# Kernel tuning notes

Hardware: AMD Instinct MI355X
Metric: run time of the kernel (lower is better)

The kernel has to match this reference:

```python
import jax, jax.numpy as jnp
import numpy as np

D = 128
N_DRUG = 100000
N_PROT = 50000
E_DD, E_DP, E_PD = 800000, 600000, 600000
EPS = 1e-5


def setup_inputs() -> dict:
    key = jax.random.key(0)
    ks = jax.random.split(key, 19)
    f32 = jnp.float32
    return {
        "x_drug": jax.random.normal(ks[0], (N_DRUG, D), f32),
        "x_prot": jax.random.normal(ks[1], (N_PROT, D), f32),
        "Wagg_dd": jax.random.normal(ks[2], (D, D), f32) * 0.05,
        "Wagg_dp": jax.random.normal(ks[3], (D, D), f32) * 0.05,
        "Wagg_pd": jax.random.normal(ks[4], (D, D), f32) * 0.05,
        "W_drug": jax.random.normal(ks[5], (D, 2 * D), f32) * 0.05,
        "b_drug": jax.random.normal(ks[6], (D,), f32) * 0.01,
        "W_prot": jax.random.normal(ks[7], (D, 2 * D), f32) * 0.05,
        "b_prot": jax.random.normal(ks[8], (D,), f32) * 0.01,
        "g_drug": jnp.ones((D,), f32),
        "be_drug": jnp.zeros((D,), f32),
        "g_prot": jnp.ones((D,), f32),
        "be_prot": jnp.zeros((D,), f32),
        "ei_dd_src": jax.random.randint(ks[9], (E_DD,), 0, N_DRUG, jnp.int64 if jax.config.jax_enable_x64 else jnp.int32),
        "ei_dd_dst": jax.random.randint(ks[10], (E_DD,), 0, N_DRUG),
        "ei_dp_src": jax.random.randint(ks[11], (E_DP,), 0, N_DRUG),
        "ei_dp_dst": jax.random.randint(ks[12], (E_DP,), 0, N_PROT),
        "ei_pd_src": jax.random.randint(ks[13], (E_PD,), 0, N_PROT),
        "ei_pd_dst": jax.random.randint(ks[14], (E_PD,), 0, N_DRUG),
    }


def _rel_agg(x_src, W_agg, src_idx, dst_idx, n_dst):
    # gather -> per-relation Linear (no bias) + ReLU -> scatter-mean
    h = jax.nn.relu(x_src[src_idx] @ W_agg.T)            # [E, D]
    s = jax.ops.segment_sum(h, dst_idx, num_segments=n_dst)
    c = jax.ops.segment_sum(jnp.ones((src_idx.shape[0],), h.dtype), dst_idx, num_segments=n_dst)
    return s / jnp.maximum(c, 1.0)[:, None]


def _layernorm(x, g, b):
    mu = jnp.mean(x, axis=-1, keepdims=True)
    var = jnp.mean(jnp.square(x - mu), axis=-1, keepdims=True)
    return (x - mu) * jax.lax.rsqrt(var + EPS) * g + b


def _node_update(h_self, h_agg, W, b, g, be):
    h = jax.nn.relu(jnp.concatenate([h_self, h_agg], axis=-1) @ W.T + b)
    return _layernorm(h + h_self, g, be)  # dropout is identity in eval


def reference(x_drug, x_prot, Wagg_dd, Wagg_dp, Wagg_pd, W_drug, b_drug,
              W_prot, b_prot, g_drug, be_drug, g_prot, be_prot,
              ei_dd_src, ei_dd_dst, ei_dp_src, ei_dp_dst, ei_pd_src, ei_pd_dst):
    agg_dd = _rel_agg(x_drug, Wagg_dd, ei_dd_src, ei_dd_dst, N_DRUG)
    agg_pd = _rel_agg(x_prot, Wagg_pd, ei_pd_src, ei_pd_dst, N_DRUG)
    agg_drug = (agg_dd + agg_pd) * 0.5                   # mean over relations into 'drug'
    agg_prot = _rel_agg(x_drug, Wagg_dp, ei_dp_src, ei_dp_dst, N_PROT)
    out_drug = _node_update(x_drug, agg_drug, W_drug, b_drug, g_drug, be_drug)
    out_prot = _node_update(x_prot, agg_prot, W_prot, b_prot, g_prot, be_prot)
    # pack the per-type outputs into one array [N_DRUG + N_PROT, D]
    return jnp.concatenate([out_drug, out_prot], axis=0)
```

## Files before the change

kernel.cpp:

```cpp
#include <hip/hip_runtime.h>

#define D 128
#define ND 100000
#define NP 50000
#define NE_DD 800000
#define NE_DP 600000
#define NE_PD 600000
#define NE_TOT 2000000

#define NTOT 250000
#define NBC 490
#define NC 250880
#define CHUNKA 4096
#define NBLKA 489
#define CHUNKIT 16
#define SEGCAP 8192

#define TF_BD 782
#define TF_BP 196
#define NU_BD 391
#define NU_BP 196

typedef __bf16 bf16;
typedef __attribute__((ext_vector_type(8))) __bf16 bf16x8;
typedef __attribute__((ext_vector_type(2))) __bf16 bf16x2;
typedef __attribute__((ext_vector_type(4))) float f32x4;
typedef __attribute__((ext_vector_type(2))) float f32x2;

#define OFF_WDD   0UL
#define OFF_WDP   32768UL
#define OFF_WPD   65536UL
#define OFF_WDRUG 98304UL
#define OFF_WPROT 163840UL
#define OFF_YDD   229376UL
#define OFF_YDP   (OFF_YDD + 25600000UL)
#define OFF_YPD   (OFF_YDP + 25600000UL)
#define OFF_AGGD  (OFF_YPD + 12800000UL)
#define OFF_AGGP  (OFF_AGGD + 25600000UL)
#define OFF_BCNT  (OFF_AGGP + 12800000UL)
#define OFF_GCUR  (OFF_BCNT + 2048UL)
#define OFF_CBASE (OFF_GCUR + 2048UL)
#define OFF_RP    (OFF_CBASE + 2048UL)
#define OFF_PAIRS (OFF_RP + 1003520UL)
#define OFF_POOL  (OFF_PAIRS + 16000000UL)

__global__ __launch_bounds__(256) void prep_kernel(
    const float* __restrict__ w0, const float* __restrict__ w1,
    const float* __restrict__ w2, const float* __restrict__ w3,
    const float* __restrict__ w4,
    bf16* __restrict__ o0, bf16* __restrict__ o1, bf16* __restrict__ o2,
    bf16* __restrict__ o3, bf16* __restrict__ o4,
    int* __restrict__ bcnt)
{
    int m = blockIdx.y;
    int i = blockIdx.x * 256 + threadIdx.x;
    if (m == 5) {
        if (i < NBC) bcnt[i] = 0;
        return;
    }
    const float* src; bf16* dst; int n; bool perm;
    switch (m) {
        case 0: src = w0; dst = o0; n = D * D; perm = false; break;
        case 1: src = w1; dst = o1; n = D * D; perm = false; break;
        case 2: src = w2; dst = o2; n = D * D; perm = false; break;
        case 3: src = w3; dst = o3; n = D * 2 * D; perm = true; break;
        default: src = w4; dst = o4; n = D * 2 * D; perm = true; break;
    }
    if (i < n) {
        int si = i;
        if (perm) {
            int col = i & 255;
            if (col >= 128) {
                int p = col - 128;
                si = (i & ~255) | (128 + (p & 7) * 16 + (p >> 3));
            }
        }
        dst[i] = (bf16)src[si];
    }
}


__device__ __forceinline__ bf16x8 load_a_f32(const float* __restrict__ xr)
{
    float4 f0 = *(const float4*)xr;
    float4 f1 = *(const float4*)(xr + 4);
    bf16x8 a;
    a[0] = (bf16)f0.x; a[1] = (bf16)f0.y; a[2] = (bf16)f0.z; a[3] = (bf16)f0.w;
    a[4] = (bf16)f1.x; a[5] = (bf16)f1.y; a[6] = (bf16)f1.z; a[7] = (bf16)f1.w;
    return a;
}

__device__ __forceinline__ void transform_drug(
    const float* __restrict__ x, const bf16* __restrict__ W1,
    const bf16* __restrict__ W2, bf16* __restrict__ y1, bf16* __restrict__ y2,
    int blk)
{
    int lane = threadIdx.x & 63;
    int wave = threadIdx.x >> 6;
    int q = lane >> 4, c = lane & 15;
    int mb = blk * 128 + wave * 32;

    f32x4 acc1[2][8], acc2[2][8];
#pragma unroll
    for (int mt = 0; mt < 2; mt++)
#pragma unroll
        for (int nt = 0; nt < 8; nt++) { acc1[mt][nt] = 0; acc2[mt][nt] = 0; }

#pragma unroll
    for (int kb = 0; kb < 4; kb++) {
        int k = kb * 32 + q * 8;
        bf16x8 a[2];
#pragma unroll
        for (int mt = 0; mt < 2; mt++) {
            int row = min(mb + mt * 16 + c, ND - 1);
            a[mt] = load_a_f32(x + (long)row * D + k);
        }
#pragma unroll
        for (int nt = 0; nt < 8; nt++) {
            bf16x8 b1 = *(const bf16x8*)(W1 + (nt * 16 + c) * D + k);
            bf16x8 b2 = *(const bf16x8*)(W2 + (nt * 16 + c) * D + k);
#pragma unroll
            for (int mt = 0; mt < 2; mt++) {
                acc1[mt][nt] = __builtin_amdgcn_mfma_f32_16x16x32_bf16(a[mt], b1, acc1[mt][nt], 0, 0, 0);
                acc2[mt][nt] = __builtin_amdgcn_mfma_f32_16x16x32_bf16(a[mt], b2, acc2[mt][nt], 0, 0, 0);
            }
        }
    }
#pragma unroll
    for (int mt = 0; mt < 2; mt++)
#pragma unroll
        for (int r = 0; r < 4; r++) {
            int row = mb + mt * 16 + q * 4 + r;
            if (row < ND) {
                bf16x8 o1, o2;
#pragma unroll
                for (int nt = 0; nt < 8; nt++) {
                    o1[nt] = (bf16)fmaxf(acc1[mt][nt][r], 0.f);
                    o2[nt] = (bf16)fmaxf(acc2[mt][nt][r], 0.f);
                }
                *(bf16x8*)(y1 + (long)row * D + c * 8) = o1;
                *(bf16x8*)(y2 + (long)row * D + c * 8) = o2;
            }
        }
}

__device__ __forceinline__ void transform_prot(
    const float* __restrict__ x, const bf16* __restrict__ W1,
    bf16* __restrict__ y1, int blk)
{
    int lane = threadIdx.x & 63;
    int wave = threadIdx.x >> 6;
    int q = lane >> 4, c = lane & 15;
    int mb = blk * 256 + wave * 64;

    f32x4 acc[4][8];
#pragma unroll
    for (int mt = 0; mt < 4; mt++)
#pragma unroll
        for (int nt = 0; nt < 8; nt++) acc[mt][nt] = 0;

#pragma unroll
    for (int kb = 0; kb < 4; kb++) {
        int k = kb * 32 + q * 8;
        bf16x8 a[4];
#pragma unroll
        for (int mt = 0; mt < 4; mt++) {
            int row = min(mb + mt * 16 + c, NP - 1);
            a[mt] = load_a_f32(x + (long)row * D + k);
        }
#pragma unroll
        for (int nt = 0; nt < 8; nt++) {
            bf16x8 b1 = *(const bf16x8*)(W1 + (nt * 16 + c) * D + k);
#pragma unroll
            for (int mt = 0; mt < 4; mt++)
                acc[mt][nt] = __builtin_amdgcn_mfma_f32_16x16x32_bf16(a[mt], b1, acc[mt][nt], 0, 0, 0);
        }
    }
#pragma unroll
    for (int mt = 0; mt < 4; mt++)
#pragma unroll
        for (int r = 0; r < 4; r++) {
            int row = mb + mt * 16 + q * 4 + r;
            if (row < NP) {
                bf16x8 o1;
#pragma unroll
                for (int nt = 0; nt < 8; nt++)
                    o1[nt] = (bf16)fmaxf(acc[mt][nt][r], 0.f);
                *(bf16x8*)(y1 + (long)row * D + c * 8) = o1;
            }
        }
}

__global__ __launch_bounds__(256, 2) void transform_kernel(
    const float* __restrict__ x_drug, const float* __restrict__ x_prot,
    const bf16* __restrict__ Wdd, const bf16* __restrict__ Wdp,
    const bf16* __restrict__ Wpd,
    bf16* __restrict__ y_dd, bf16* __restrict__ y_dp, bf16* __restrict__ y_pd)
{
    int blk = blockIdx.x;
    if (blk < TF_BD)
        transform_drug(x_drug, Wdd, Wdp, y_dd, y_dp, blk);
    else
        transform_prot(x_prot, Wpd, y_pd, blk - TF_BD);
}

__global__ __launch_bounds__(256) void hist_kernel(
    const int* __restrict__ dd_dst, const int* __restrict__ pd_dst,
    const int* __restrict__ dp_dst, int* __restrict__ bcnt)
{
    __shared__ int h[NBC];
    for (int i = threadIdx.x; i < NBC; i += 256) h[i] = 0;
    __syncthreads();
    int base = blockIdx.x * CHUNKA;
    for (int it = 0; it < CHUNKIT; it++) {
        int e = base + it * 256 + threadIdx.x;
        if (e < NE_TOT) {
            int didx;
            if (e < NE_DD) didx = dd_dst[e];
            else if (e < NE_DD + NE_PD) didx = ND + pd_dst[e - NE_DD];
            else didx = 2 * ND + dp_dst[e - NE_DD - NE_PD];
            atomicAdd(&h[didx >> 9], 1);
        }
    }
    __syncthreads();
    for (int i = threadIdx.x; i < NBC; i += 256)
        if (h[i]) atomicAdd(&bcnt[i], h[i]);
}

__global__ __launch_bounds__(256) void scan_kernel(
    const int* __restrict__ bcnt, int* __restrict__ cbase, int* __restrict__ gcur)
{
    __shared__ int ps[256];
    int t = threadIdx.x;
    int i0 = 2 * t, i1 = 2 * t + 1;
    int c0 = (i0 < NBC) ? bcnt[i0] : 0;
    int c1 = (i1 < NBC) ? bcnt[i1] : 0;
    ps[t] = c0 + c1;
    __syncthreads();
#pragma unroll
    for (int off = 1; off < 256; off <<= 1) {
        int add = (t >= off) ? ps[t - off] : 0;
        __syncthreads();
        ps[t] += add;
        __syncthreads();
    }
    int excl = ps[t] - (c0 + c1);
    if (i0 <= NBC) cbase[i0] = excl;
    if (i0 < NBC) gcur[i0] = excl;
    if (i1 < NBC) { cbase[i1] = excl + c0; gcur[i1] = excl + c0; }
}

__global__ __launch_bounds__(256) void binA_kernel(
    const int* __restrict__ dd_src, const int* __restrict__ dd_dst,
    const int* __restrict__ pd_src, const int* __restrict__ pd_dst,
    const int* __restrict__ dp_src, const int* __restrict__ dp_dst,
    int* __restrict__ gcur, int2* __restrict__ pairs)
{
    __shared__ int h[NBC];
    __shared__ int gb[NBC];
    __shared__ int2 pr[CHUNKA];
    __shared__ unsigned short rk[CHUNKA];
    for (int i = threadIdx.x; i < NBC; i += 256) h[i] = 0;
    __syncthreads();
    int base = blockIdx.x * CHUNKA;
    for (int it = 0; it < CHUNKIT; it++) {
        int idx = it * 256 + threadIdx.x;
        int e = base + idx;
        int didx = -1, sv = 0;
        if (e < NE_TOT) {
            if (e < NE_DD) { didx = dd_dst[e]; sv = dd_src[e]; }
            else if (e < NE_DD + NE_PD) { int u = e - NE_DD; didx = ND + pd_dst[u]; sv = pd_src[u]; }
            else { int u = e - NE_DD - NE_PD; didx = 2 * ND + dp_dst[u]; sv = dp_src[u]; }
            rk[idx] = (unsigned short)atomicAdd(&h[didx >> 9], 1);
        }
        pr[idx] = make_int2(didx, sv);
    }
    __syncthreads();
    for (int b = threadIdx.x; b < NBC; b += 256) {
        int c = h[b];
        gb[b] = c ? atomicAdd(&gcur[b], c) : 0;
    }
    __syncthreads();
    for (int it = 0; it < CHUNKIT; it++) {
        int idx = it * 256 + threadIdx.x;
        int2 p = pr[idx];
        if (p.x >= 0) pairs[gb[p.x >> 9] + rk[idx]] = p;
    }
}

__global__ __launch_bounds__(256) void sortB_kernel(
    const int* __restrict__ cbase, const int2* __restrict__ pairs,
    int* __restrict__ pool, int* __restrict__ rp)
{
    __shared__ int h[512];
    __shared__ int excl[512];
    __shared__ int ps[256];
    __shared__ unsigned short rk[SEGCAP];
    __shared__ int outl[SEGCAP];

    int b = blockIdx.x;
    int s0 = cbase[b], s1 = cbase[b + 1];
    int n = s1 - s0;
    if (n > SEGCAP) n = SEGCAP;
    int t = threadIdx.x;
    h[t] = 0; h[t + 256] = 0;
    __syncthreads();

    for (int i = t; i < n; i += 256) {
        int2 p = pairs[s0 + i];
        rk[i] = (unsigned short)atomicAdd(&h[p.x & 511], 1);
    }
    __syncthreads();

    int c0 = h[2 * t], c1 = h[2 * t + 1];
    ps[t] = c0 + c1;
    __syncthreads();
#pragma unroll
    for (int off = 1; off < 256; off <<= 1) {
        int add = (t >= off) ? ps[t - off] : 0;
        __syncthreads();
        ps[t] += add;
        __syncthreads();
    }
    int pe = ps[t] - (c0 + c1);
    excl[2 * t] = pe;
    excl[2 * t + 1] = pe + c0;
    __syncthreads();

    int nb = b * 512;
    rp[nb + 2 * t] = s0 + excl[2 * t];
    rp[nb + 2 * t + 1] = s0 + excl[2 * t + 1];

    for (int i = t; i < n; i += 256) {
        int2 p = pairs[s0 + i];
        outl[excl[p.x & 511] + rk[i]] = p.y;
    }
    __syncthreads();
    for (int i = t; i < n; i += 256)
        pool[s0 + i] = outl[i];
}

__device__ __forceinline__ void acc2(unsigned u, f32x2* acc)
{
    union { unsigned u; float f; } lo, hi;
    lo.u = u << 16;
    hi.u = u & 0xFFFF0000u;
    f32x2 d; d.x = lo.f; d.y = hi.f;
    *acc += d;
}

__device__ __forceinline__ void acc_seg(
    const int* __restrict__ pool, int s, int e,
    const unsigned* __restrict__ y, int lane, f32x2* acc)
{
    int j = s;
    for (; j + 8 <= e; j += 8) {
        unsigned u[8];
#pragma unroll
        for (int t = 0; t < 8; t++)
            u[t] = y[(long)pool[j + t] * 64 + lane];
#pragma unroll
        for (int t = 0; t < 8; t++) acc2(u[t], acc);
    }
    if (j + 4 <= e) {
        unsigned u[4];
#pragma unroll
        for (int t = 0; t < 4; t++)
            u[t] = y[(long)pool[j + t] * 64 + lane];
#pragma unroll
        for (int t = 0; t < 4; t++) acc2(u[t], acc);
        j += 4;
    }
    if (j + 2 <= e) {
        unsigned u0 = y[(long)pool[j] * 64 + lane];
        unsigned u1 = y[(long)pool[j + 1] * 64 + lane];
        acc2(u0, acc); acc2(u1, acc);
        j += 2;
    }
    if (j < e)
        acc2(y[(long)pool[j] * 64 + lane], acc);
}

__global__ __launch_bounds__(256) void gather_kernel(
    const int* __restrict__ rp, const int* __restrict__ pool,
    const unsigned* __restrict__ y_dd, const unsigned* __restrict__ y_pd,
    const unsigned* __restrict__ y_dp,
    bf16* __restrict__ agg_d, bf16* __restrict__ agg_p)
{
    int wid = blockIdx.x * 4 + (threadIdx.x >> 6);
    int lane = threadIdx.x & 63;

    if (wid < ND) {
        int g = wid;
        int s1 = rp[g], e1 = rp[g + 1];
        int s2 = rp[ND + g], e2 = rp[ND + g + 1];
        f32x2 a; a.x = 0.f; a.y = 0.f;
        f32x2 b; b.x = 0.f; b.y = 0.f;
        acc_seg(pool, s1, e1, y_dd, lane, &a);
        acc_seg(pool, s2, e2, y_pd, lane, &b);
        float i1 = 0.5f / (float)max(e1 - s1, 1);
        float i2 = 0.5f / (float)max(e2 - s2, 1);
        f32x2 r = a * i1 + b * i2;
        bf16x2 o; o[0] = (bf16)r.x; o[1] = (bf16)r.y;
        *(bf16x2*)(agg_d + (long)g * D + lane * 2) = o;
    } else if (wid < ND + NP) {
        int p = wid - ND;
        int s1 = rp[2 * ND + p], e1 = rp[2 * ND + p + 1];
        f32x2 a; a.x = 0.f; a.y = 0.f;
        acc_seg(pool, s1, e1, y_dp, lane, &a);
        float i1 = 1.0f / (float)max(e1 - s1, 1);
        f32x2 r = a * i1;
        bf16x2 o; o[0] = (bf16)r.x; o[1] = (bf16)r.y;
        *(bf16x2*)(agg_p + (long)p * D + lane * 2) = o;
    }
}

__device__ __forceinline__ void node_update_body(
    const float* __restrict__ x, const bf16* __restrict__ agg,
    const bf16* __restrict__ W, const float* __restrict__ b,
    const float* __restrict__ g, const float* __restrict__ be,
    float* __restrict__ out, int M, int blk)
{
    int lane = threadIdx.x & 63;
    int wave = threadIdx.x >> 6;
    int q = lane >> 4, c = lane & 15;
    int mb = blk * 256 + wave * 64;

    f32x4 acc[4][8];
#pragma unroll
    for (int mt = 0; mt < 4; mt++)
#pragma unroll
        for (int nt = 0; nt < 8; nt++) acc[mt][nt] = 0;

#pragma unroll
    for (int kb = 0; kb < 8; kb++) {
        bf16x8 a[4];
#pragma unroll
        for (int mt = 0; mt < 4; mt++) {
            int row = min(mb + mt * 16 + c, M - 1);
            if (kb < 4)
                a[mt] = load_a_f32(x + (long)row * D + kb * 32 + q * 8);
            else
                a[mt] = *(const bf16x8*)(agg + (long)row * D + (kb - 4) * 32 + q * 8);
        }
#pragma unroll
        for (int nt = 0; nt < 8; nt++) {
            bf16x8 bw = *(const bf16x8*)(W + (nt * 16 + c) * (2 * D) + kb * 32 + q * 8);
#pragma unroll
            for (int mt = 0; mt < 4; mt++)
                acc[mt][nt] = __builtin_amdgcn_mfma_f32_16x16x32_bf16(a[mt], bw, acc[mt][nt], 0, 0, 0);
        }
    }

    float bv[8], gv[8], bev[8];
#pragma unroll
    for (int nt = 0; nt < 8; nt++) {
        int col = nt * 16 + c;
        bv[nt] = b[col]; gv[nt] = g[col]; bev[nt] = be[col];
    }
#pragma unroll
    for (int mt = 0; mt < 4; mt++)
#pragma unroll
        for (int r = 0; r < 4; r++) {
            int row = mb + mt * 16 + q * 4 + r;
            int rowc = min(row, M - 1);
            const float* xr = x + (long)rowc * D + c;
            float v[8];
            float sum = 0.f, sq = 0.f;
#pragma unroll
            for (int nt = 0; nt < 8; nt++) {
                float h = fmaxf(acc[mt][nt][r] + bv[nt], 0.f);
                float t = h + xr[nt * 16];
                v[nt] = t; sum += t; sq += t * t;
            }
#pragma unroll
            for (int m = 1; m < 16; m <<= 1) {
                sum += __shfl_xor(sum, m, 64);
                sq  += __shfl_xor(sq,  m, 64);
            }
            float mu   = sum * (1.f / 128.f);
            float var  = sq  * (1.f / 128.f) - mu * mu;
            float rstd = rsqrtf(var + 1e-5f);
            if (row < M) {
                float* op = out + (long)row * D + c;
#pragma unroll
                for (int nt = 0; nt < 8; nt++)
                    op[nt * 16] = (v[nt] - mu) * rstd * gv[nt] + bev[nt];
            }
        }
}

__global__ __launch_bounds__(256, 2) void node_update_kernel(
    const float* __restrict__ x_drug, const float* __restrict__ x_prot,
    const bf16* __restrict__ agg_d, const bf16* __restrict__ agg_p,
    const bf16* __restrict__ Wdrug, const float* __restrict__ b_drug,
    const float* __restrict__ g_drug, const float* __restrict__ be_drug,
    const bf16* __restrict__ Wprot, const float* __restrict__ b_prot,
    const float* __restrict__ g_prot, const float* __restrict__ be_prot,
    float* __restrict__ out)
{
    int blk = blockIdx.x;
    if (blk < NU_BD)
        node_update_body(x_drug, agg_d, Wdrug, b_drug, g_drug, be_drug,
                         out, ND, blk);
    else
        node_update_body(x_prot, agg_p, Wprot, b_prot, g_prot, be_prot,
                         out + (long)ND * D, NP, blk - NU_BD);
}

extern "C" void kernel_launch(void* const* d_in, const int* in_sizes, int n_in,
                              void* d_out, int out_size, void* d_ws, size_t ws_size,
                              hipStream_t stream)
{
    const float* x_drug  = (const float*)d_in[0];
    const float* x_prot  = (const float*)d_in[1];
    const float* Wagg_dd = (const float*)d_in[2];
    const float* Wagg_dp = (const float*)d_in[3];
    const float* Wagg_pd = (const float*)d_in[4];
    const float* W_drug  = (const float*)d_in[5];
    const float* b_drug  = (const float*)d_in[6];
    const float* W_prot  = (const float*)d_in[7];
    const float* b_prot  = (const float*)d_in[8];
    const float* g_drug  = (const float*)d_in[9];
    const float* be_drug = (const float*)d_in[10];
    const float* g_prot  = (const float*)d_in[11];
    const float* be_prot = (const float*)d_in[12];
    const int* dd_src = (const int*)d_in[13];
    const int* dd_dst = (const int*)d_in[14];
    const int* dp_src = (const int*)d_in[15];
    const int* dp_dst = (const int*)d_in[16];
    const int* pd_src = (const int*)d_in[17];
    const int* pd_dst = (const int*)d_in[18];

    char* ws = (char*)d_ws;
    bf16* Wdd   = (bf16*)(ws + OFF_WDD);
    bf16* Wdp   = (bf16*)(ws + OFF_WDP);
    bf16* Wpd   = (bf16*)(ws + OFF_WPD);
    bf16* Wdrug = (bf16*)(ws + OFF_WDRUG);
    bf16* Wprot = (bf16*)(ws + OFF_WPROT);
    bf16* y_dd  = (bf16*)(ws + OFF_YDD);
    bf16* y_dp  = (bf16*)(ws + OFF_YDP);
    bf16* y_pd  = (bf16*)(ws + OFF_YPD);
    bf16* agg_d = (bf16*)(ws + OFF_AGGD);
    bf16* agg_p = (bf16*)(ws + OFF_AGGP);
    int* bcnt   = (int*)(ws + OFF_BCNT);
    int* gcur   = (int*)(ws + OFF_GCUR);
    int* cbase  = (int*)(ws + OFF_CBASE);
    int* rp     = (int*)(ws + OFF_RP);
    int2* pairs = (int2*)(ws + OFF_PAIRS);
    int* pool   = (int*)(ws + OFF_POOL);
    float* out  = (float*)d_out;

    prep_kernel<<<dim3(128, 6), 256, 0, stream>>>(
        Wagg_dd, Wagg_dp, Wagg_pd, W_drug, W_prot,
        Wdd, Wdp, Wpd, Wdrug, Wprot, bcnt);

    transform_kernel<<<TF_BD + TF_BP, 256, 0, stream>>>(
        x_drug, x_prot, Wdd, Wdp, Wpd, y_dd, y_dp, y_pd);

    hist_kernel<<<NBLKA, 256, 0, stream>>>(dd_dst, pd_dst, dp_dst, bcnt);
    scan_kernel<<<1, 256, 0, stream>>>(bcnt, cbase, gcur);
    binA_kernel<<<NBLKA, 256, 0, stream>>>(
        dd_src, dd_dst, pd_src, pd_dst, dp_src, dp_dst, gcur, pairs);
    sortB_kernel<<<NBC, 256, 0, stream>>>(cbase, pairs, pool, rp);

    gather_kernel<<<(ND + NP + 3) / 4, 256, 0, stream>>>(
        rp, pool, (const unsigned*)y_dd, (const unsigned*)y_pd,
        (const unsigned*)y_dp, agg_d, agg_p);

    node_update_kernel<<<NU_BD + NU_BP, 256, 0, stream>>>(
        x_drug, x_prot, agg_d, agg_p,
        Wdrug, b_drug, g_drug, be_drug,
        Wprot, b_prot, g_prot, be_prot, out);
}
```

Baseline: 404.3 us.

## Fuse histogram into prep, co-schedule binning with transform, pack edge pairs

Moves the destination-bucket histogram into the weight-prep kernel (using a grid-stride loop over 128 blocks) and zeroes the bucket counts with a memset. The binning pass and the MFMA feature transform now run as one heterogeneous launch so the memory-bound binning overlaps the compute-bound transform. Edge pairs are packed into a single 32-bit word (low 9 bits of the destination plus a 17-bit source index) instead of int2, halving the intermediate pair traffic. This removes two kernel launches and their serialization, but the shared-memory footprint of the fused kernel may limit occupancy for the transform blocks.

```diff
diff --git a/kernel.cpp b/kernel.cpp
--- a/kernel.cpp
+++ b/kernel.cpp
@@ -50,14 +50,28 @@
     const float* __restrict__ w4,
     bf16* __restrict__ o0, bf16* __restrict__ o1, bf16* __restrict__ o2,
     bf16* __restrict__ o3, bf16* __restrict__ o4,
-    int* __restrict__ bcnt)
+    const int* __restrict__ dd_dst, const int* __restrict__ pd_dst,
+    const int* __restrict__ dp_dst, int* __restrict__ bcnt)
 {
     int m = blockIdx.y;
-    int i = blockIdx.x * 256 + threadIdx.x;
+    int t = threadIdx.x;
     if (m == 5) {
-        if (i < NBC) bcnt[i] = 0;
+        __shared__ int h[NBC];
+        for (int i = t; i < NBC; i += 256) h[i] = 0;
+        __syncthreads();
+        for (int e = blockIdx.x * 256 + t; e < NE_TOT; e += 128 * 256) {
+            int didx;
+            if (e < NE_DD) didx = dd_dst[e];
+            else if (e < NE_DD + NE_PD) didx = ND + pd_dst[e - NE_DD];
+            else didx = 2 * ND + dp_dst[e - NE_DD - NE_PD];
+            atomicAdd(&h[didx >> 9], 1);
+        }
+        __syncthreads();
+        for (int i = t; i < NBC; i += 256)
+            if (h[i]) atomicAdd(&bcnt[i], h[i]);
         return;
     }
+    int i = blockIdx.x * 256 + t;
     const float* src; bf16* dst; int n; bool perm;
     switch (m) {
         case 0: src = w0; dst = o0; n = D * D; perm = false; break;
@@ -79,6 +93,28 @@
     }
 }
 
+__global__ __launch_bounds__(256) void scan_kernel(
+    const int* __restrict__ bcnt, int* __restrict__ cbase, int* __restrict__ gcur)
+{
+    __shared__ int ps[256];
+    int t = threadIdx.x;
+    int i0 = 2 * t, i1 = 2 * t + 1;
+    int c0 = (i0 < NBC) ? bcnt[i0] : 0;
+    int c1 = (i1 < NBC) ? bcnt[i1] : 0;
+    ps[t] = c0 + c1;
+    __syncthreads();
+#pragma unroll
+    for (int off = 1; off < 256; off <<= 1) {
+        int add = (t >= off) ? ps[t - off] : 0;
+        __syncthreads();
+        ps[t] += add;
+        __syncthreads();
+    }
+    int excl = ps[t] - (c0 + c1);
+    if (i0 <= NBC) cbase[i0] = excl;
+    if (i0 < NBC) gcur[i0] = excl;
+    if (i1 < NBC) { cbase[i1] = excl + c0; gcur[i1] = excl + c0; }
+}
 
 __device__ __forceinline__ bf16x8 load_a_f32(const float* __restrict__ xr)
 {
@@ -191,70 +227,12 @@
         }
 }
 
-__global__ __launch_bounds__(256, 2) void transform_kernel(
-    const float* __restrict__ x_drug, const float* __restrict__ x_prot,
-    const bf16* __restrict__ Wdd, const bf16* __restrict__ Wdp,
-    const bf16* __restrict__ Wpd,
-    bf16* __restrict__ y_dd, bf16* __restrict__ y_dp, bf16* __restrict__ y_pd)
-{
-    int blk = blockIdx.x;
-    if (blk < TF_BD)
-        transform_drug(x_drug, Wdd, Wdp, y_dd, y_dp, blk);
-    else
-        transform_prot(x_prot, Wpd, y_pd, blk - TF_BD);
-}
-
-__global__ __launch_bounds__(256) void hist_kernel(
-    const int* __restrict__ dd_dst, const int* __restrict__ pd_dst,
-    const int* __restrict__ dp_dst, int* __restrict__ bcnt)
-{
-    __shared__ int h[NBC];
-    for (int i = threadIdx.x; i < NBC; i += 256) h[i] = 0;
-    __syncthreads();
-    int base = blockIdx.x * CHUNKA;
-    for (int it = 0; it < CHUNKIT; it++) {
-        int e = base + it * 256 + threadIdx.x;
-        if (e < NE_TOT) {
-            int didx;
-            if (e < NE_DD) didx = dd_dst[e];
-            else if (e < NE_DD + NE_PD) didx = ND + pd_dst[e - NE_DD];
-            else didx = 2 * ND + dp_dst[e - NE_DD - NE_PD];
-            atomicAdd(&h[didx >> 9], 1);
-        }
-    }
-    __syncthreads();
-    for (int i = threadIdx.x; i < NBC; i += 256)
-        if (h[i]) atomicAdd(&bcnt[i], h[i]);
-}
-
-__global__ __launch_bounds__(256) void scan_kernel(
-    const int* __restrict__ bcnt, int* __restrict__ cbase, int* __restrict__ gcur)
-{
-    __shared__ int ps[256];
-    int t = threadIdx.x;
-    int i0 = 2 * t, i1 = 2 * t + 1;
-    int c0 = (i0 < NBC) ? bcnt[i0] : 0;
-    int c1 = (i1 < NBC) ? bcnt[i1] : 0;
-    ps[t] = c0 + c1;
-    __syncthreads();
-#pragma unroll
-    for (int off = 1; off < 256; off <<= 1) {
-        int add = (t >= off) ? ps[t - off] : 0;
-        __syncthreads();
-        ps[t] += add;
-        __syncthreads();
-    }
-    int excl = ps[t] - (c0 + c1);
-    if (i0 <= NBC) cbase[i0] = excl;
-    if (i0 < NBC) gcur[i0] = excl;
-    if (i1 < NBC) { cbase[i1] = excl + c0; gcur[i1] = excl + c0; }
-}
-
-__global__ __launch_bounds__(256) void binA_kernel(
+__device__ __forceinline__ void binA_body(
+    int blk,
     const int* __restrict__ dd_src, const int* __restrict__ dd_dst,
     const int* __restrict__ pd_src, const int* __restrict__ pd_dst,
     const int* __restrict__ dp_src, const int* __restrict__ dp_dst,
-    int* __restrict__ gcur, int2* __restrict__ pairs)
+    int* __restrict__ gcur, unsigned* __restrict__ pairs)
 {
     __shared__ int h[NBC];
     __shared__ int gb[NBC];
@@ -262,7 +240,7 @@
     __shared__ unsigned short rk[CHUNKA];
     for (int i = threadIdx.x; i < NBC; i += 256) h[i] = 0;
     __syncthreads();
-    int base = blockIdx.x * CHUNKA;
+    int base = blk * CHUNKA;
     for (int it = 0; it < CHUNKIT; it++) {
         int idx = it * 256 + threadIdx.x;
         int e = base + idx;
@@ -284,12 +262,37 @@
     for (int it = 0; it < CHUNKIT; it++) {
         int idx = it * 256 + threadIdx.x;
         int2 p = pr[idx];
-        if (p.x >= 0) pairs[gb[p.x >> 9] + rk[idx]] = p;
-    }
+        if (p.x >= 0)
+            pairs[gb[p.x >> 9] + rk[idx]] =
+                ((unsigned)(p.x & 511) << 17) | (unsigned)p.y;
+    }
+}
+
+__global__ __launch_bounds__(256, 2) void stage2_kernel(
+    const float* __restrict__ x_drug, const float* __restrict__ x_prot,
+    const bf16* __restrict__ Wdd, const bf16* __restrict__ Wdp,
+    const bf16* __restrict__ Wpd,
+    bf16* __restrict__ y_dd, bf16* __restrict__ y_dp, bf16* __restrict__ y_pd,
+    const int* __restrict__ dd_src, const int* __restrict__ dd_dst,
+    const int* __restrict__ pd_src, const int* __restrict__ pd_dst,
+    const int* __restrict__ dp_src, const int* __restrict__ dp_dst,
+    int* __restrict__ gcur, unsigned* __restrict__ pairs)
+{
+    int blk = blockIdx.x;
+    if (blk < NBLKA) {
+        binA_body(blk, dd_src, dd_dst, pd_src, pd_dst, dp_src, dp_dst,
+                  gcur, pairs);
+        return;
+    }
+    blk -= NBLKA;
+    if (blk < TF_BD)
+        transform_drug(x_drug, Wdd, Wdp, y_dd, y_dp, blk);
+    else
+        transform_prot(x_prot, Wpd, y_pd, blk - TF_BD);
 }
 
 __global__ __launch_bounds__(256) void sortB_kernel(
-    const int* __restrict__ cbase, const int2* __restrict__ pairs,
+    const int* __restrict__ cbase, const unsigned* __restrict__ pairs,
     int* __restrict__ pool, int* __restrict__ rp)
 {
     __shared__ int h[512];
@@ -307,8 +310,8 @@
     __syncthreads();
 
     for (int i = t; i < n; i += 256) {
-        int2 p = pairs[s0 + i];
-        rk[i] = (unsigned short)atomicAdd(&h[p.x & 511], 1);
+        unsigned p = pairs[s0 + i];
+        rk[i] = (unsigned short)atomicAdd(&h[p >> 17], 1);
     }
     __syncthreads();
 
@@ -332,8 +335,8 @@
     rp[nb + 2 * t + 1] = s0 + excl[2 * t + 1];
 
     for (int i = t; i < n; i += 256) {
-        int2 p = pairs[s0 + i];
-        outl[excl[p.x & 511] + rk[i]] = p.y;
+        unsigned p = pairs[s0 + i];
+        outl[excl[p >> 17] + rk[i]] = (int)(p & 0x1FFFFu);
     }
     __syncthreads();
     for (int i = t; i < n; i += 256)
@@ -547,21 +550,23 @@
     int* gcur   = (int*)(ws + OFF_GCUR);
     int* cbase  = (int*)(ws + OFF_CBASE);
     int* rp     = (int*)(ws + OFF_RP);
-    int2* pairs = (int2*)(ws + OFF_PAIRS);
+    unsigned* pairs = (unsigned*)(ws + OFF_PAIRS);
     int* pool   = (int*)(ws + OFF_POOL);
     float* out  = (float*)d_out;
 
+    hipMemsetAsync(bcnt, 0, NBC * sizeof(int), stream);
+
     prep_kernel<<<dim3(128, 6), 256, 0, stream>>>(
         Wagg_dd, Wagg_dp, Wagg_pd, W_drug, W_prot,
-        Wdd, Wdp, Wpd, Wdrug, Wprot, bcnt);
-
-    transform_kernel<<<TF_BD + TF_BP, 256, 0, stream>>>(
-        x_drug, x_prot, Wdd, Wdp, Wpd, y_dd, y_dp, y_pd);
-
-    hist_kernel<<<NBLKA, 256, 0, stream>>>(dd_dst, pd_dst, dp_dst, bcnt);
+        Wdd, Wdp, Wpd, Wdrug, Wprot,
+        dd_dst, pd_dst, dp_dst, bcnt);
+
     scan_kernel<<<1, 256, 0, stream>>>(bcnt, cbase, gcur);
-    binA_kernel<<<NBLKA, 256, 0, stream>>>(
+
+    stage2_kernel<<<NBLKA + TF_BD + TF_BP, 256, 0, stream>>>(
+        x_drug, x_prot, Wdd, Wdp, Wpd, y_dd, y_dp, y_pd,
         dd_src, dd_dst, pd_src, pd_dst, dp_src, dp_dst, gcur, pairs);
+
     sortB_kernel<<<NBC, 256, 0, stream>>>(cbase, pairs, pool, rp);
 
     gather_kernel<<<(ND + NP + 3) / 4, 256, 0, stream>>>(
```

Measured after the change: 416.0 us. 1.03x slower.
